# Optimization experiments

Measured on AMD Instinct MI355X. Metric: run time of the kernel, lower is better.

The kernel has to match this reference:

```python
import jax, jax.numpy as jnp
import numpy as np

B, F0, K = 256, 40, 32          # batch, num fields, embedding dim
CIN_SIZE = [200, 200]            # layer widths (field_num[1:])


def setup_inputs() -> dict:
    key = jax.random.key(0)
    ks = jax.random.split(key, 1 + 4 * len(CIN_SIZE))
    field_num = [F0] + CIN_SIZE
    d = {"inputs": jax.random.normal(ks[0], (B, F0, K), dtype=jnp.float32)}
    for i in range(len(CIN_SIZE)):
        # W_query: (1, Fi, K); W_key/W_value: (1, F0, K); cin_W: (1, F0*Fi, F_{i+1})
        d[f"wq{i}"] = jax.random.normal(ks[1 + 4 * i], (1, field_num[i], K), dtype=jnp.float32) * 0.05
        d[f"wk{i}"] = jax.random.normal(ks[2 + 4 * i], (1, F0, K), dtype=jnp.float32) * 0.05
        d[f"wv{i}"] = jax.random.normal(ks[3 + 4 * i], (1, F0, K), dtype=jnp.float32) * 0.05
        lim = (6.0 / (F0 * field_num[i] + field_num[i + 1])) ** 0.5  # glorot uniform
        d[f"cw{i}"] = jax.random.uniform(ks[4 + 4 * i], (1, F0 * field_num[i], field_num[i + 1]),
                                         minval=-lim, maxval=lim, dtype=jnp.float32)
    return d


def _cin(inputs, params):
    # inputs: [B, F0, K]; params: list of (wq, wk, wv, cw) per CIN layer
    Bb, F0_, Kk = inputs.shape
    res = inputs
    outs = []
    for (wq, wk, wv, cw) in params:
        x0_wk = inputs * wk                 # [B, F0, K]
        x0_wv = inputs * wv                 # [B, F0, K]
        xi_wq = res * wq                    # [B, Fi, K]
        # per-embedding-slot outer product scores: phi[b,k,f0,fi]
        phi = jnp.einsum('bfk,bgk->bkfg', x0_wk, xi_wq)
        # exp + normalize over F0 axis == softmax over axis=2
        alpha = jax.nn.softmax(phi, axis=2)                      # [B, K, F0, Fi]
        x = alpha * jnp.transpose(x0_wv, (0, 2, 1))[:, :, :, None]  # [B, K, F0, Fi]
        x = x.reshape(Bb, Kk, -1)           # flatten (f0, fi) row-major -> f0*Fi + fi
        # conv1d with kernel width 1 == channel matmul: [B, K, F0*Fi] @ [F0*Fi, F_{i+1}]
        out = jnp.einsum('bkc,cj->bjk', x, cw[0])                # [B, F_{i+1}, K]
        outs.append(out)
        res = out
    cat = jnp.concatenate(outs, axis=1)     # [B, sum(cin_size), K]
    return cat.sum(axis=-1)                 # [B, sum(cin_size)]


def reference(inputs, wq0, wk0, wv0, cw0, wq1, wk1, wv1, cw1):
    return _cin(inputs, [(wq0, wk0, wv0, cw0), (wq1, wk1, wv1, cw1)])
```

## Files before the change

### kernel.cpp

```cpp
#include <hip/hip_runtime.h>
#include <hip/hip_bf16.h>


#define NF0   40
#define KD    32
#define NJ    200
#define NTILE 14
#define NTHR  512

typedef short bf16x8 __attribute__((ext_vector_type(8)));
typedef float f32x4  __attribute__((ext_vector_type(4)));
typedef unsigned short u16;
typedef unsigned int   u32;
typedef unsigned long long u64;

static __device__ __forceinline__ u16 f2bf(float f) {
    __hip_bfloat16 h = __float2bfloat16(f);
    return *reinterpret_cast<u16*>(&h);
}
static __device__ __forceinline__ float bf2f(u16 u) {
    u32 x = ((u32)u) << 16;
    float f;
    __builtin_memcpy(&f, &x, 4);
    return f;
}

template<int FI>
__global__ __launch_bounds__(256)
void pack_b(const float* __restrict__ cw, u16* __restrict__ bp, int G) {
    __shared__ float tile[64][17];
    const int band = blockIdx.x, nt = blockIdx.y;
    const int t = threadIdx.x;
    {
        const int cl = t >> 2, qj = t & 3;
        const int cp = band * 64 + cl;
        const int fi = cp / NF0, f0 = cp - fi * NF0;
        const int j0 = nt * 16 + qj * 4;
        float4 v = make_float4(0.f, 0.f, 0.f, 0.f);
        if (fi < FI) {
            const float* src = cw + (size_t)(f0 * FI + fi) * NJ + j0;
            if (j0 + 3 < NJ) v = *reinterpret_cast<const float4*>(src);
            else {
                if (j0 + 0 < NJ) v.x = src[0];
                if (j0 + 1 < NJ) v.y = src[1];
                if (j0 + 2 < NJ) v.z = src[2];
                if (j0 + 3 < NJ) v.w = src[3];
            }
        }
        tile[cl][qj * 4 + 0] = v.x;
        tile[cl][qj * 4 + 1] = v.y;
        tile[cl][qj * 4 + 2] = v.z;
        tile[cl][qj * 4 + 3] = v.w;
    }
    __syncthreads();
    if (t < 128) {
        const int g2 = t >> 6, lane = t & 63;
        const int jl = lane & 15, c8 = g2 * 32 + (lane >> 4) * 8;
        u16 v[8];
        #pragma unroll
        for (int i = 0; i < 8; ++i) v[i] = f2bf(tile[c8 + i][jl]);
        *reinterpret_cast<bf16x8*>(bp + ((size_t)(nt * G + band * 2 + g2) * 64 + lane) * 8)
            = *reinterpret_cast<const bf16x8*>(v);
    }
}

__global__ __launch_bounds__(NTHR, 4)
void cin_layer0(const float* __restrict__ x0,
                const float* __restrict__ wq, const float* __restrict__ wk,
                const float* __restrict__ wv,
                const u16* __restrict__ bp, u16* __restrict__ res) {
    constexpr int G0 = 50;
    __shared__ float s_xk[1280], s_xv[1280], s_q[1280];
    __shared__ u16 s_XT[32 * 384];

    const int tid = threadIdx.x;
    const int b = blockIdx.x >> 1, js = blockIdx.x & 1;
    const int wid = tid >> 6, lane = tid & 63;
    const int wrow = lane & 15, wq4 = lane >> 4;
    const int mg = wid & 1, ng = wid >> 1;

    for (int i = tid; i < 1280; i += NTHR) {
        float v = x0[(size_t)b * 1280 + i];
        s_xk[i] = v * wk[i];
        s_xv[i] = v * wv[i];
        s_q[i]  = v * wq[i];
    }
    __syncthreads();

    f32x4 acc[2];
    #pragma unroll
    for (int t = 0; t < 2; ++t) acc[t] = (f32x4){0.f, 0.f, 0.f, 0.f};

    const int sfil = tid >> 6, sh = (tid >> 5) & 1, sk = tid & 31;
    char* srb = (char*)s_XT + sk * 768;
    const int sswx = (sk & 7) << 4;
    const int arow = mg * 16 + wrow;
    char* apb = (char*)s_XT + arow * 768;
    const int aswx = (arow & 7) << 4;

    for (int ch = 0; ch < 5; ++ch) {
        {
            const float qv = s_q[(ch * 8 + sfil) * 32 + sk];
            const float* xkp = s_xk + sh * 640 + sk;
            const float* xvp = s_xv + sh * 640 + sk;
            float e[20];
            float d = 0.f;
            #pragma unroll
            for (int i = 0; i < 20; ++i) {
                e[i] = __expf(xkp[i * 32] * qv);
                d += e[i];
            }
            d += __shfl_xor(d, 32);
            const float r = 1.0f / d;
            #pragma unroll
            for (int p = 0; p < 10; ++p) {
                u32 w = (u32)f2bf(e[2 * p] * r * xvp[(2 * p) * 32])
                      | ((u32)f2bf(e[2 * p + 1] * r * xvp[(2 * p + 1) * 32]) << 16);
                *reinterpret_cast<u32*>(srb + ((sfil * 80 + sh * 40 + p * 4) ^ sswx)) = w;
            }
        }
        __syncthreads();
        __builtin_amdgcn_s_setprio(1);
        #pragma unroll
        for (int ks = 0; ks < 10; ++ks) {
            bf16x8 a = *reinterpret_cast<const bf16x8*>(apb + ((ks * 64 + wq4 * 16) ^ aswx));
            const int g = ch * 10 + ks;
            #pragma unroll
            for (int t = 0; t < 2; ++t) {
                const int ntl = ng * 2 + t;
                if (ntl < 7) {
                    const int nt = js * 7 + ntl;
                    bf16x8 bfr = *reinterpret_cast<const bf16x8*>(
                        bp + ((size_t)(nt * G0 + g) * 64 + lane) * 8);
                    acc[t] = __builtin_amdgcn_mfma_f32_16x16x32_bf16(a, bfr, acc[t], 0, 0, 0);
                }
            }
        }
        __builtin_amdgcn_s_setprio(0);
        __syncthreads();
    }

    const int kbase = mg * 16 + wq4 * 4;
    #pragma unroll
    for (int t = 0; t < 2; ++t) {
        const int ntl = ng * 2 + t;
        if (ntl < 7) {
            const int j = (js * 7 + ntl) * 16 + wrow;
            if (j < NJ) {
                u16 pk[4];
                #pragma unroll
                for (int r = 0; r < 4; ++r) pk[r] = f2bf(acc[t][r]);
                *reinterpret_cast<u64*>(res + (size_t)b * (NJ * KD) + j * KD + kbase)
                    = *reinterpret_cast<const u64*>(pk);
            }
        }
    }
}

__global__ __launch_bounds__(NTHR, 4)
void cin_layer1(const float* __restrict__ x0, const u16* __restrict__ resb,
                const float* __restrict__ wq, const float* __restrict__ wk,
                const float* __restrict__ wv,
                const u16* __restrict__ bp, float* __restrict__ out) {
    constexpr int G1 = 260, FIR = 52;
    __shared__ float s_xk[2560], s_xv[2560], s_q[2 * FIR * 32];
    __shared__ u16 s_XT[64 * 192];

    const int tid = threadIdx.x;
    const int bg = blockIdx.x >> 2, split = blockIdx.x & 3;
    const int b0 = bg * 2;
    const int wid = tid >> 6, lane = tid & 63;
    const int wrow = lane & 15, wq4 = lane >> 4;
    const int mg = wid & 3, ng = wid >> 2;

    if (split == 0) {
        for (int idx = tid; idx < 2 * NJ; idx += NTHR) {
            const int bb = idx / NJ, j = idx - bb * NJ;
            const u16* rp = resb + (size_t)(b0 + bb) * (NJ * KD) + j * KD;
            float s = 0.f;
            #pragma unroll
            for (int q8 = 0; q8 < 4; ++q8) {
                bf16x8 v = *reinterpret_cast<const bf16x8*>(rp + q8 * 8);
                #pragma unroll
                for (int i = 0; i < 8; ++i) s += bf2f((u16)v[i]);
            }
            out[(size_t)(b0 + bb) * 400 + j] = s;
        }
    }

    for (int idx = tid; idx < 2560; idx += NTHR) {
        const int bb = idx / 1280, r = idx - bb * 1280;
        float v = x0[(size_t)(b0 + bb) * 1280 + r];
        s_xk[idx] = v * wk[r];
        s_xv[idx] = v * wv[r];
    }
    for (int idx = tid; idx < 2 * FIR * 32; idx += NTHR) {
        const int bb = idx / (FIR * 32), rr = idx - bb * (FIR * 32);
        const int fi = split * FIR + (rr >> 5), k = rr & 31;
        float qv = 0.f;
        if (fi < 200)
            qv = bf2f(resb[(size_t)(b0 + bb) * (NJ * KD) + fi * KD + k]) * wq[fi * KD + k];
        s_q[idx] = qv;
    }
    __syncthreads();

    f32x4 acc[7];
    #pragma unroll
    for (int t = 0; t < 7; ++t) acc[t] = (f32x4){0.f, 0.f, 0.f, 0.f};

    const int sbb = tid >> 8, sfil = (tid >> 6) & 3, sh = (tid >> 5) & 1, sk = tid & 31;
    const int srow = sbb * 32 + sk;
    char* srb = (char*)s_XT + srow * 384;
    const int sswx = (srow & 7) << 4;
    const int arow = mg * 16 + wrow;
    char* apb = (char*)s_XT + arow * 384;
    const int aswx = (arow & 7) << 4;

    for (int ch = 0; ch < 13; ++ch) {
        const int fig = split * FIR + ch * 4 + sfil;
        if (fig < 200) {
            const float qv = s_q[sbb * (FIR * 32) + (ch * 4 + sfil) * 32 + sk];
            const float* xkp = s_xk + sbb * 1280 + sh * 640 + sk;
            const float* xvp = s_xv + sbb * 1280 + sh * 640 + sk;
            float e[20];
            float d = 0.f;
            #pragma unroll
            for (int i = 0; i < 20; ++i) {
                e[i] = __expf(xkp[i * 32] * qv);
                d += e[i];
            }
            d += __shfl_xor(d, 32);
            const float r = 1.0f / d;
            #pragma unroll
            for (int p = 0; p < 10; ++p) {
                u32 w = (u32)f2bf(e[2 * p] * r * xvp[(2 * p) * 32])
                      | ((u32)f2bf(e[2 * p + 1] * r * xvp[(2 * p + 1) * 32]) << 16);
                *reinterpret_cast<u32*>(srb + ((sfil * 80 + sh * 40 + p * 4) ^ sswx)) = w;
            }
        } else {
            #pragma unroll
            for (int p = 0; p < 10; ++p)
                *reinterpret_cast<u32*>(srb + ((sfil * 80 + sh * 40 + p * 4) ^ sswx)) = 0u;
        }
        __syncthreads();
        __builtin_amdgcn_s_setprio(1);
        #pragma unroll
        for (int ks = 0; ks < 5; ++ks) {
            bf16x8 a = *reinterpret_cast<const bf16x8*>(apb + ((ks * 64 + wq4 * 16) ^ aswx));
            const int g = split * 65 + ch * 5 + ks;
            #pragma unroll
            for (int t = 0; t < 7; ++t) {
                const int nt2 = ng * 7 + t;
                bf16x8 bfr = *reinterpret_cast<const bf16x8*>(
                    bp + ((size_t)(nt2 * G1 + g) * 64 + lane) * 8);
                acc[t] = __builtin_amdgcn_mfma_f32_16x16x32_bf16(a, bfr, acc[t], 0, 0, 0);
            }
        }
        __builtin_amdgcn_s_setprio(0);
        __syncthreads();
    }

    #pragma unroll
    for (int t = 0; t < 7; ++t) {
        float s = acc[t][0] + acc[t][1] + acc[t][2] + acc[t][3];
        s += __shfl_xor(s, 16);
        s += __shfl_xor(s, 32);
        const int j = (ng * 7 + t) * 16 + wrow;
        if (wq4 == 0 && j < NJ) {
            const int bb = mg >> 1;
            atomicAdd(&out[(size_t)(b0 + bb) * 400 + 200 + j], s);
        }
    }
}

extern "C" void kernel_launch(void* const* d_in, const int* in_sizes, int n_in,
                              void* d_out, int out_size, void* d_ws, size_t ws_size,
                              hipStream_t stream) {
    const float* x0  = (const float*)d_in[0];
    const float* wq0 = (const float*)d_in[1];
    const float* wk0 = (const float*)d_in[2];
    const float* wv0 = (const float*)d_in[3];
    const float* cw0 = (const float*)d_in[4];
    const float* wq1 = (const float*)d_in[5];
    const float* wk1 = (const float*)d_in[6];
    const float* wv1 = (const float*)d_in[7];
    const float* cw1 = (const float*)d_in[8];
    float* out = (float*)d_out;

    char* ws = (char*)d_ws;
    u16* res = (u16*)ws;
    u16* bp0 = (u16*)(ws + 3276800);
    u16* bp1 = (u16*)(ws + 3276800 + 716800);

    hipMemsetAsync(d_out, 0, (size_t)out_size * 4, stream);

    pack_b<40> <<<dim3(25, NTILE), 256, 0, stream>>>(cw0, bp0, 50);
    pack_b<200><<<dim3(130, NTILE), 256, 0, stream>>>(cw1, bp1, 260);

    cin_layer0<<<512, NTHR, 0, stream>>>(x0, wq0, wk0, wv0, bp0, res);
    cin_layer1<<<512, NTHR, 0, stream>>>(x0, res, wq1, wk1, wv1, bp1, out);
}
```

Before: 199.8 us.

## Switch CIN matmuls to 32x32x16 MFMA with split-K layer0 partial outputs

Both layer kernels move from 16x16x32 to 32x32x16 bf16 MFMA tiles, and the packed weight layout is regenerated to 32-column tiles. Layer 0 now splits the reduction over Fi halves instead of splitting output columns, writing two partial result buffers that layer 1 sums when it reads them. The xk/xv rows are hoisted into registers, and LDS writes are widened to 64-bit. The aim is fewer MFMA issues and B-fragment loads per FLOP. The cost is a doubled intermediate buffer and extra reads, and in layer 0 only 4 of 8 waves do the softmax while 7 do the MFMA.

After: 187.6 us. -6.1%, faster.

```diff
diff --git a/kernel.cpp b/kernel.cpp
--- a/kernel.cpp
+++ b/kernel.cpp
@@ -2,14 +2,13 @@
 #include <hip/hip_bf16.h>
 
 
-#define NF0   40
-#define KD    32
-#define NJ    200
-#define NTILE 14
-#define NTHR  512
+#define NF0  40
+#define KD   32
+#define NJ   200
+#define NTHR 512
 
 typedef short bf16x8 __attribute__((ext_vector_type(8)));
-typedef float f32x4  __attribute__((ext_vector_type(4)));
+typedef float f32x16 __attribute__((ext_vector_type(16)));
 typedef unsigned short u16;
 typedef unsigned int   u32;
 typedef unsigned long long u64;
@@ -28,38 +27,33 @@
 template<int FI>
 __global__ __launch_bounds__(256)
 void pack_b(const float* __restrict__ cw, u16* __restrict__ bp, int G) {
-    __shared__ float tile[64][17];
-    const int band = blockIdx.x, nt = blockIdx.y;
-    const int t = threadIdx.x;
-    {
-        const int cl = t >> 2, qj = t & 3;
-        const int cp = band * 64 + cl;
-        const int fi = cp / NF0, f0 = cp - fi * NF0;
-        const int j0 = nt * 16 + qj * 4;
+    __shared__ u16 s[160][33];
+    const int fi0 = blockIdx.x * 4;
+    const int nt  = blockIdx.y;
+    const int t   = threadIdx.x;
+    #pragma unroll
+    for (int it = 0; it < 5; ++it) {
+        int idx = it * 256 + t;
+        int rl = idx >> 3, q4 = idx & 7;
+        int f0 = rl >> 2, fl = rl & 3;
+        int fi = fi0 + fl;
+        int j0 = nt * 32 + q4 * 4;
         float4 v = make_float4(0.f, 0.f, 0.f, 0.f);
-        if (fi < FI) {
-            const float* src = cw + (size_t)(f0 * FI + fi) * NJ + j0;
-            if (j0 + 3 < NJ) v = *reinterpret_cast<const float4*>(src);
-            else {
-                if (j0 + 0 < NJ) v.x = src[0];
-                if (j0 + 1 < NJ) v.y = src[1];
-                if (j0 + 2 < NJ) v.z = src[2];
-                if (j0 + 3 < NJ) v.w = src[3];
-            }
-        }
-        tile[cl][qj * 4 + 0] = v.x;
-        tile[cl][qj * 4 + 1] = v.y;
-        tile[cl][qj * 4 + 2] = v.z;
-        tile[cl][qj * 4 + 3] = v.w;
+        if (fi < FI && j0 <= NJ - 4)
+            v = *reinterpret_cast<const float4*>(cw + (size_t)(f0 * FI + fi) * NJ + j0);
+        int cl = fl * 40 + f0;
+        s[cl][q4 * 4 + 0] = f2bf(v.x);
+        s[cl][q4 * 4 + 1] = f2bf(v.y);
+        s[cl][q4 * 4 + 2] = f2bf(v.z);
+        s[cl][q4 * 4 + 3] = f2bf(v.w);
     }
     __syncthreads();
-    if (t < 128) {
-        const int g2 = t >> 6, lane = t & 63;
-        const int jl = lane & 15, c8 = g2 * 32 + (lane >> 4) * 8;
+    for (int ft = t; ft < 640; ft += 256) {
+        int g = ft >> 6, l = ft & 63;
         u16 v[8];
         #pragma unroll
-        for (int i = 0; i < 8; ++i) v[i] = f2bf(tile[c8 + i][jl]);
-        *reinterpret_cast<bf16x8*>(bp + ((size_t)(nt * G + band * 2 + g2) * 64 + lane) * 8)
+        for (int i = 0; i < 8; ++i) v[i] = s[g * 16 + 8 * (l >> 5) + i][l & 31];
+        *reinterpret_cast<bf16x8*>(bp + ((size_t)(nt * G + blockIdx.x * 10 + g) * 64 + l) * 8)
             = *reinterpret_cast<const bf16x8*>(v);
     }
 }
@@ -68,121 +62,115 @@
 void cin_layer0(const float* __restrict__ x0,
                 const float* __restrict__ wq, const float* __restrict__ wk,
                 const float* __restrict__ wv,
-                const u16* __restrict__ bp, u16* __restrict__ res) {
-    constexpr int G0 = 50;
-    __shared__ float s_xk[1280], s_xv[1280], s_q[1280];
-    __shared__ u16 s_XT[32 * 384];
-
+                const u16* __restrict__ bp, u16* __restrict__ resp) {
+    __shared__ float s_xk[1280], s_xv[1280], s_q[640];
+    __shared__ u64 s_XT[32 * 48];
     const int tid = threadIdx.x;
-    const int b = blockIdx.x >> 1, js = blockIdx.x & 1;
+    const int b = blockIdx.x >> 1, half = blockIdx.x & 1;
     const int wid = tid >> 6, lane = tid & 63;
-    const int wrow = lane & 15, wq4 = lane >> 4;
-    const int mg = wid & 1, ng = wid >> 1;
+    const int jcol = lane & 31, hh = lane >> 5;
 
     for (int i = tid; i < 1280; i += NTHR) {
         float v = x0[(size_t)b * 1280 + i];
         s_xk[i] = v * wk[i];
         s_xv[i] = v * wv[i];
-        s_q[i]  = v * wq[i];
+    }
+    for (int i = tid; i < 640; i += NTHR) {
+        int fi = half * 20 + (i >> 5), k = i & 31;
+        s_q[i] = x0[(size_t)b * 1280 + fi * 32 + k] * wq[fi * 32 + k];
     }
     __syncthreads();
 
-    f32x4 acc[2];
-    #pragma unroll
-    for (int t = 0; t < 2; ++t) acc[t] = (f32x4){0.f, 0.f, 0.f, 0.f};
-
-    const int sfil = tid >> 6, sh = (tid >> 5) & 1, sk = tid & 31;
-    char* srb = (char*)s_XT + sk * 768;
-    const int sswx = (sk & 7) << 4;
-    const int arow = mg * 16 + wrow;
-    char* apb = (char*)s_XT + arow * 768;
-    const int aswx = (arow & 7) << 4;
+    const int sk = lane & 31, sh = lane >> 5, sfil = wid;
+    float xkr[20], xvr[20];
+    if (wid < 4) {
+        #pragma unroll
+        for (int i = 0; i < 20; ++i) {
+            xkr[i] = s_xk[(sh * 20 + i) * 32 + sk];
+            xvr[i] = s_xv[(sh * 20 + i) * 32 + sk];
+        }
+    }
+
+    f32x16 acc;
+    #pragma unroll
+    for (int r = 0; r < 16; ++r) acc[r] = 0.f;
+    const int nt = wid;
+    char* aptr = (char*)s_XT + jcol * 384;
+    const int aswz = (jcol & 7) << 4;
 
     for (int ch = 0; ch < 5; ++ch) {
-        {
-            const float qv = s_q[(ch * 8 + sfil) * 32 + sk];
-            const float* xkp = s_xk + sh * 640 + sk;
-            const float* xvp = s_xv + sh * 640 + sk;
-            float e[20];
-            float d = 0.f;
-            #pragma unroll
-            for (int i = 0; i < 20; ++i) {
-                e[i] = __expf(xkp[i * 32] * qv);
-                d += e[i];
-            }
+        if (wid < 4) {
+            const float q = s_q[(ch * 4 + sfil) * 32 + sk];
+            float e[20], d = 0.f;
+            #pragma unroll
+            for (int i = 0; i < 20; ++i) { e[i] = __expf(xkr[i] * q); d += e[i]; }
             d += __shfl_xor(d, 32);
-            const float r = 1.0f / d;
-            #pragma unroll
-            for (int p = 0; p < 10; ++p) {
-                u32 w = (u32)f2bf(e[2 * p] * r * xvp[(2 * p) * 32])
-                      | ((u32)f2bf(e[2 * p + 1] * r * xvp[(2 * p + 1) * 32]) << 16);
-                *reinterpret_cast<u32*>(srb + ((sfil * 80 + sh * 40 + p * 4) ^ sswx)) = w;
+            const float rr = 1.0f / d;
+            char* rb = (char*)s_XT + sk * 384;
+            const int swz = (sk & 7) << 4;
+            #pragma unroll
+            for (int p = 0; p < 5; ++p) {
+                u64 w = (u64)f2bf(e[4*p+0] * rr * xvr[4*p+0])
+                      | ((u64)f2bf(e[4*p+1] * rr * xvr[4*p+1]) << 16)
+                      | ((u64)f2bf(e[4*p+2] * rr * xvr[4*p+2]) << 32)
+                      | ((u64)f2bf(e[4*p+3] * rr * xvr[4*p+3]) << 48);
+                *reinterpret_cast<u64*>(rb + ((sfil * 80 + sh * 40 + p * 8) ^ swz)) = w;
             }
         }
         __syncthreads();
         __builtin_amdgcn_s_setprio(1);
-        #pragma unroll
-        for (int ks = 0; ks < 10; ++ks) {
-            bf16x8 a = *reinterpret_cast<const bf16x8*>(apb + ((ks * 64 + wq4 * 16) ^ aswx));
-            const int g = ch * 10 + ks;
-            #pragma unroll
-            for (int t = 0; t < 2; ++t) {
-                const int ntl = ng * 2 + t;
-                if (ntl < 7) {
-                    const int nt = js * 7 + ntl;
-                    bf16x8 bfr = *reinterpret_cast<const bf16x8*>(
-                        bp + ((size_t)(nt * G0 + g) * 64 + lane) * 8);
-                    acc[t] = __builtin_amdgcn_mfma_f32_16x16x32_bf16(a, bfr, acc[t], 0, 0, 0);
-                }
+        if (wid < 7) {
+            #pragma unroll
+            for (int ks = 0; ks < 10; ++ks) {
+                bf16x8 a = *reinterpret_cast<const bf16x8*>(aptr + ((ks * 32 + hh * 16) ^ aswz));
+                const int g = half * 50 + ch * 10 + ks;
+                bf16x8 bf = *reinterpret_cast<const bf16x8*>(
+                    bp + ((size_t)(nt * 100 + g) * 64 + lane) * 8);
+                acc = __builtin_amdgcn_mfma_f32_32x32x16_bf16(a, bf, acc, 0, 0, 0);
             }
         }
         __builtin_amdgcn_s_setprio(0);
         __syncthreads();
     }
 
-    const int kbase = mg * 16 + wq4 * 4;
-    #pragma unroll
-    for (int t = 0; t < 2; ++t) {
-        const int ntl = ng * 2 + t;
-        if (ntl < 7) {
-            const int j = (js * 7 + ntl) * 16 + wrow;
-            if (j < NJ) {
-                u16 pk[4];
-                #pragma unroll
-                for (int r = 0; r < 4; ++r) pk[r] = f2bf(acc[t][r]);
-                *reinterpret_cast<u64*>(res + (size_t)b * (NJ * KD) + j * KD + kbase)
-                    = *reinterpret_cast<const u64*>(pk);
+    if (wid < 7) {
+        const int j = nt * 32 + jcol;
+        if (j < NJ) {
+            u16* dst = resp + (size_t)(half * 256 + b) * 6400 + j * 32;
+            #pragma unroll
+            for (int rg = 0; rg < 4; ++rg) {
+                u64 w = (u64)f2bf(acc[4*rg+0]) | ((u64)f2bf(acc[4*rg+1]) << 16)
+                      | ((u64)f2bf(acc[4*rg+2]) << 32) | ((u64)f2bf(acc[4*rg+3]) << 48);
+                *reinterpret_cast<u64*>(dst + 8 * rg + 4 * hh) = w;
             }
         }
     }
 }
 
 __global__ __launch_bounds__(NTHR, 4)
-void cin_layer1(const float* __restrict__ x0, const u16* __restrict__ resb,
+void cin_layer1(const float* __restrict__ x0, const u16* __restrict__ resp,
                 const float* __restrict__ wq, const float* __restrict__ wk,
                 const float* __restrict__ wv,
                 const u16* __restrict__ bp, float* __restrict__ out) {
-    constexpr int G1 = 260, FIR = 52;
-    __shared__ float s_xk[2560], s_xv[2560], s_q[2 * FIR * 32];
-    __shared__ u16 s_XT[64 * 192];
-
+    __shared__ float s_xk[2560], s_xv[2560], s_q[3328];
+    __shared__ u64 s_XT[64 * 48];
     const int tid = threadIdx.x;
     const int bg = blockIdx.x >> 2, split = blockIdx.x & 3;
     const int b0 = bg * 2;
     const int wid = tid >> 6, lane = tid & 63;
-    const int wrow = lane & 15, wq4 = lane >> 4;
-    const int mg = wid & 3, ng = wid >> 2;
 
     if (split == 0) {
         for (int idx = tid; idx < 2 * NJ; idx += NTHR) {
             const int bb = idx / NJ, j = idx - bb * NJ;
-            const u16* rp = resb + (size_t)(b0 + bb) * (NJ * KD) + j * KD;
+            const u16* r0 = resp + (size_t)(b0 + bb) * 6400 + j * 32;
+            const u16* r1 = resp + (size_t)(256 + b0 + bb) * 6400 + j * 32;
             float s = 0.f;
             #pragma unroll
             for (int q8 = 0; q8 < 4; ++q8) {
-                bf16x8 v = *reinterpret_cast<const bf16x8*>(rp + q8 * 8);
+                bf16x8 v0 = *reinterpret_cast<const bf16x8*>(r0 + q8 * 8);
+                bf16x8 v1 = *reinterpret_cast<const bf16x8*>(r1 + q8 * 8);
                 #pragma unroll
-                for (int i = 0; i < 8; ++i) s += bf2f((u16)v[i]);
+                for (int i = 0; i < 8; ++i) s += bf2f((u16)v0[i]) + bf2f((u16)v1[i]);
             }
             out[(size_t)(b0 + bb) * 400 + j] = s;
         }
@@ -194,66 +182,78 @@
         s_xk[idx] = v * wk[r];
         s_xv[idx] = v * wv[r];
     }
-    for (int idx = tid; idx < 2 * FIR * 32; idx += NTHR) {
-        const int bb = idx / (FIR * 32), rr = idx - bb * (FIR * 32);
-        const int fi = split * FIR + (rr >> 5), k = rr & 31;
+    for (int idx = tid; idx < 3328; idx += NTHR) {
+        const int bb = idx / 1664, rr = idx - bb * 1664;
+        const int fi = split * 52 + (rr >> 5), k = rr & 31;
         float qv = 0.f;
-        if (fi < 200)
-            qv = bf2f(resb[(size_t)(b0 + bb) * (NJ * KD) + fi * KD + k]) * wq[fi * KD + k];
+        if (fi < 200) {
+            float rv = bf2f(resp[(size_t)(b0 + bb) * 6400 + fi * 32 + k])
+                     + bf2f(resp[(size_t)(256 + b0 + bb) * 6400 + fi * 32 + k]);
+            qv = rv * wq[fi * 32 + k];
+        }
         s_q[idx] = qv;
     }
     __syncthreads();
 
-    f32x4 acc[7];
-    #pragma unroll
-    for (int t = 0; t < 7; ++t) acc[t] = (f32x4){0.f, 0.f, 0.f, 0.f};
-
-    const int sbb = tid >> 8, sfil = (tid >> 6) & 3, sh = (tid >> 5) & 1, sk = tid & 31;
+    const int sbb = wid >> 2, sfil = wid & 3, sh = lane >> 5, sk = lane & 31;
     const int srow = sbb * 32 + sk;
+    float xkr[20], xvr[20];
+    #pragma unroll
+    for (int i = 0; i < 20; ++i) {
+        xkr[i] = s_xk[sbb * 1280 + (sh * 20 + i) * 32 + sk];
+        xvr[i] = s_xv[sbb * 1280 + (sh * 20 + i) * 32 + sk];
+    }
     char* srb = (char*)s_XT + srow * 384;
-    const int sswx = (srow & 7) << 4;
-    const int arow = mg * 16 + wrow;
-    char* apb = (char*)s_XT + arow * 384;
-    const int aswx = (arow & 7) << 4;
+    const int sswz = (srow & 7) << 4;
+
+    const int mg = wid & 1, ng = wid >> 1;
+    const int nt0 = ng, nt1 = ng + 4;
+    const int ntc = (ng < 3) ? 2 : 1;
+    f32x16 acc[2];
+    #pragma unroll
+    for (int t = 0; t < 2; ++t)
+        #pragma unroll
+        for (int r = 0; r < 16; ++r) acc[t][r] = 0.f;
+    const int arow = mg * 32 + (lane & 31);
+    char* aptr = (char*)s_XT + arow * 384;
+    const int aswz = (arow & 7) << 4;
+    const int ah = (lane >> 5) * 16;
 
     for (int ch = 0; ch < 13; ++ch) {
-        const int fig = split * FIR + ch * 4 + sfil;
+        const int fig = split * 52 + ch * 4 + sfil;
         if (fig < 200) {
-            const float qv = s_q[sbb * (FIR * 32) + (ch * 4 + sfil) * 32 + sk];
-            const float* xkp = s_xk + sbb * 1280 + sh * 640 + sk;
-            const float* xvp = s_xv + sbb * 1280 + sh * 640 + sk;
-            float e[20];
-            float d = 0.f;
-            #pragma unroll
-            for (int i = 0; i < 20; ++i) {
-                e[i] = __expf(xkp[i * 32] * qv);
-                d += e[i];
-            }
+            const float q = s_q[sbb * 1664 + (ch * 4 + sfil) * 32 + sk];
+            float e[20], d = 0.f;
+            #pragma unroll
+            for (int i = 0; i < 20; ++i) { e[i] = __expf(xkr[i] * q); d += e[i]; }
             d += __shfl_xor(d, 32);
-            const float r = 1.0f / d;
-            #pragma unroll
-            for (int p = 0; p < 10; ++p) {
-                u32 w = (u32)f2bf(e[2 * p] * r * xvp[(2 * p) * 32])
-                      | ((u32)f2bf(e[2 * p + 1] * r * xvp[(2 * p + 1) * 32]) << 16);
-                *reinterpret_cast<u32*>(srb + ((sfil * 80 + sh * 40 + p * 4) ^ sswx)) = w;
+            const float rr = 1.0f / d;
+            #pragma unroll
+            for (int p = 0; p < 5; ++p) {
+                u64 w = (u64)f2bf(e[4*p+0] * rr * xvr[4*p+0])
+                      | ((u64)f2bf(e[4*p+1] * rr * xvr[4*p+1]) << 16)
+                      | ((u64)f2bf(e[4*p+2] * rr * xvr[4*p+2]) << 32)
+                      | ((u64)f2bf(e[4*p+3] * rr * xvr[4*p+3]) << 48);
+                *reinterpret_cast<u64*>(srb + ((sfil * 80 + sh * 40 + p * 8) ^ sswz)) = w;
             }
         } else {
             #pragma unroll
-            for (int p = 0; p < 10; ++p)
-                *reinterpret_cast<u32*>(srb + ((sfil * 80 + sh * 40 + p * 4) ^ sswx)) = 0u;
+            for (int p = 0; p < 5; ++p)
+                *reinterpret_cast<u64*>(srb + ((sfil * 80 + sh * 40 + p * 8) ^ sswz)) = 0ull;
         }
         __syncthreads();
         __builtin_amdgcn_s_setprio(1);
         #pragma unroll
-        for (int ks = 0; ks < 5; ++ks) {
-            bf16x8 a = *reinterpret_cast<const bf16x8*>(apb + ((ks * 64 + wq4 * 16) ^ aswx));
-            const int g = split * 65 + ch * 5 + ks;
-            #pragma unroll
-            for (int t = 0; t < 7; ++t) {
-                const int nt2 = ng * 7 + t;
-                bf16x8 bfr = *reinterpret_cast<const bf16x8*>(
-                    bp + ((size_t)(nt2 * G1 + g) * 64 + lane) * 8);
-                acc[t] = __builtin_amdgcn_mfma_f32_16x16x32_bf16(a, bfr, acc[t], 0, 0, 0);
+        for (int ks = 0; ks < 10; ++ks) {
+            bf16x8 a = *reinterpret_cast<const bf16x8*>(aptr + ((ks * 32 + ah) ^ aswz));
+            const int g = split * 130 + ch * 10 + ks;
+            bf16x8 bf0 = *reinterpret_cast<const bf16x8*>(
+                bp + ((size_t)(nt0 * 520 + g) * 64 + lane) * 8);
+            acc[0] = __builtin_amdgcn_mfma_f32_32x32x16_bf16(a, bf0, acc[0], 0, 0, 0);
+            if (ntc == 2) {
+                bf16x8 bf1 = *reinterpret_cast<const bf16x8*>(
+                    bp + ((size_t)(nt1 * 520 + g) * 64 + lane) * 8);
+                acc[1] = __builtin_amdgcn_mfma_f32_32x32x16_bf16(a, bf1, acc[1], 0, 0, 0);
             }
         }
         __builtin_amdgcn_s_setprio(0);
@@ -261,14 +261,16 @@
     }
 
     #pragma unroll
-    for (int t = 0; t < 7; ++t) {
-        float s = acc[t][0] + acc[t][1] + acc[t][2] + acc[t][3];
-        s += __shfl_xor(s, 16);
-        s += __shfl_xor(s, 32);
-        const int j = (ng * 7 + t) * 16 + wrow;
-        if (wq4 == 0 && j < NJ) {
-            const int bb = mg >> 1;
-            atomicAdd(&out[(size_t)(b0 + bb) * 400 + 200 + j], s);
+    for (int t = 0; t < 2; ++t) {
+        if (t < ntc) {
+            float s = 0.f;
+            #pragma unroll
+            for (int r = 0; r < 16; ++r) s += acc[t][r];
+            s += __shfl_xor(s, 32);
+            const int nt = (t == 0) ? nt0 : nt1;
+            const int j = nt * 32 + (lane & 31);
+            if (lane < 32 && j < NJ)
+                atomicAdd(&out[(size_t)(b0 + mg) * 400 + 200 + j], s);
         }
     }
 }
@@ -288,15 +290,15 @@
     float* out = (float*)d_out;
 
     char* ws = (char*)d_ws;
-    u16* res = (u16*)ws;
-    u16* bp0 = (u16*)(ws + 3276800);
-    u16* bp1 = (u16*)(ws + 3276800 + 716800);
+    u16* resp = (u16*)ws;
+    u16* bp0  = (u16*)(ws + 6553600);
+    u16* bp1  = (u16*)(ws + 6553600 + 716800);
 
     hipMemsetAsync(d_out, 0, (size_t)out_size * 4, stream);
 
-    pack_b<40> <<<dim3(25, NTILE), 256, 0, stream>>>(cw0, bp0, 50);
-    pack_b<200><<<dim3(130, NTILE), 256, 0, stream>>>(cw1, bp1, 260);
-
-    cin_layer0<<<512, NTHR, 0, stream>>>(x0, wq0, wk0, wv0, bp0, res);
-    cin_layer1<<<512, NTHR, 0, stream>>>(x0, res, wq1, wk1, wv1, bp1, out);
-}
+    pack_b<40> <<<dim3(10, 7), 256, 0, stream>>>(cw0, bp0, 100);
+    pack_b<200><<<dim3(52, 7), 256, 0, stream>>>(cw1, bp1, 520);
+
+    cin_layer0<<<512, NTHR, 0, stream>>>(x0, wq0, wk0, wv0, bp0, resp);
+    cin_layer1<<<512, NTHR, 0, stream>>>(x0, resp, wq1, wk1, wv1, bp1, out);
+}
```
